# Kernel tuning notes

Measured on AMD Instinct MI355X. Metric: run time of the kernel, lower is better.

Reference implementation:

```python
import jax, jax.numpy as jnp
import numpy as np

DIM = 384
NUM_HEADS = 12
HEAD_DIM = 32
MID = NUM_HEADS * HEAD_DIM
RES = (32, 32)


def _relative_position_index(res):
    Hh, Ww = res
    coords = np.stack(np.meshgrid(np.arange(Hh), np.arange(Ww), indexing='ij'))  # 2,H,W
    cf = coords.reshape(2, -1)
    rel = cf[:, :, None] - cf[:, None, :]  # 2,N,N
    rel = rel.transpose(1, 2, 0).astype(np.int64)
    rel[:, :, 0] += Hh - 1
    rel[:, :, 1] += Ww - 1
    rel[:, :, 0] *= 2 * Ww - 1
    return rel.sum(-1)  # N,N


def setup_inputs() -> dict:
    key = jax.random.key(0)
    ks = jax.random.split(key, 8)
    B = 8
    Hh, Ww = RES
    table_size = (2 * Hh - 1) * (2 * Ww - 1)
    x = jax.random.normal(ks[0], (B, DIM, Hh, Ww), dtype=jnp.float32)
    wq = jax.random.normal(ks[1], (MID, DIM), dtype=jnp.float32) * 0.02
    bq = jnp.zeros((MID,), dtype=jnp.float32)
    wkv = jax.random.normal(ks[2], (2 * MID, DIM), dtype=jnp.float32) * 0.02
    bkv = jnp.zeros((2 * MID,), dtype=jnp.float32)
    wproj = jax.random.normal(ks[3], (DIM, MID), dtype=jnp.float32) * 0.02
    bproj = jnp.zeros((DIM,), dtype=jnp.float32)
    bias_table = jax.random.normal(ks[4], (table_size, NUM_HEADS), dtype=jnp.float32) * 0.02
    rel_index = jnp.asarray(_relative_position_index(RES), dtype=jnp.int32)  # N,N
    return {"x": x, "wq": wq, "bq": bq, "wkv": wkv, "bkv": bkv,
            "wproj": wproj, "bproj": bproj, "bias_table": bias_table,
            "rel_index": rel_index}


def reference(x, wq, bq, wkv, bkv, wproj, bproj, bias_table, rel_index):
    B, C, Hh, Ww = x.shape
    N = Hh * Ww
    scale = HEAD_DIM ** -0.5
    xf = x.reshape(B, C, N)  # B,C,N
    # 1x1 convs == channelwise linear
    q = jnp.einsum('oc,bcn->bon', wq, xf) + bq[None, :, None]          # B,MID,N
    kv = jnp.einsum('oc,bcn->bon', wkv, xf) + bkv[None, :, None]       # B,2*MID,N
    q = q.reshape(B, NUM_HEADS, HEAD_DIM, N).transpose(0, 1, 3, 2)     # B,h,N,d
    kv = kv.reshape(B, 2, NUM_HEADS, HEAD_DIM, N)
    k = kv[:, 0].transpose(0, 1, 3, 2)                                  # B,h,N,d
    v = kv[:, 1].transpose(0, 1, 3, 2)                                  # B,h,N,d
    attn = jnp.einsum('bhnd,bhmd->bhnm', q, k) * scale                  # B,h,N,N
    rel_bias = bias_table[rel_index.reshape(-1)].reshape(N, N, NUM_HEADS)
    attn = attn + rel_bias.transpose(2, 0, 1)[None]                     # + h,N,N bias
    attn = jax.nn.softmax(attn, axis=-1)
    out = jnp.einsum('bhnm,bhmd->bhnd', attn, v)                        # B,h,N,d
    out = out.transpose(0, 1, 3, 2).reshape(B, MID, N)                  # B,MID,N
    out = jnp.einsum('om,bmn->bon', wproj, out) + bproj[None, :, None]  # B,DIM,N
    return out.reshape(B, C, Hh, Ww)
```

## Files before the change

kernel.cpp:

```cpp
#include <hip/hip_runtime.h>

typedef __bf16 bf16;
typedef __bf16 bf16x8 __attribute__((ext_vector_type(8)));
typedef __bf16 bf16x4 __attribute__((ext_vector_type(4)));
typedef float  f32x4  __attribute__((ext_vector_type(4)));

static constexpr int NB = 8;
static constexpr int NH = 12;
static constexpr int HD = 32;
static constexpr int NN = 1024;
static constexpr int NC = 384;
static constexpr int NTBL = 3969;

static constexpr float LOG2E = 1.4426950408889634f;
static constexpr float QSC   = (float)(0.17677669529663687 * 1.4426950408889634);

static constexpr size_t XT_N   = (size_t)NB*NN*NC;
static constexpr size_t WQKV_N = (size_t)3*NC*NC;
static constexpr size_t WP_N   = (size_t)NC*NC;
static constexpr size_t QKV_N  = (size_t)NB*NH*NN*HD;

static constexpr size_t XT_OFF   = 0;
static constexpr size_t WQKV_OFF = XT_OFF + XT_N;
static constexpr size_t WP_OFF   = WQKV_OFF + WQKV_N;
static constexpr size_t Q_OFF    = WP_OFF + WP_N;
static constexpr size_t K_OFF    = Q_OFF + QKV_N;
static constexpr size_t V_OFF    = K_OFF + QKV_N;
static constexpr size_t AO_OFF   = V_OFF + QKV_N;

#define MFMA16(a,b,c) __builtin_amdgcn_mfma_f32_16x16x32_bf16(a,b,c,0,0,0)

static __device__ inline float fast_exp2(float x) {
#if __has_builtin(__builtin_amdgcn_exp2f)
    return __builtin_amdgcn_exp2f(x);
#else
    return exp2f(x);
#endif
}

__global__ __launch_bounds__(256) void cast_all_kernel(const float* __restrict__ x,
                                                       const float* __restrict__ wq,
                                                       const float* __restrict__ wkv,
                                                       const float* __restrict__ wproj,
                                                       bf16* __restrict__ xt,
                                                       bf16* __restrict__ wqkv,
                                                       bf16* __restrict__ wp)
{
    __shared__ bf16 T[64][68];
    const int t = threadIdx.x;
    if (blockIdx.x >= 768) {
        const size_t i = ((size_t)(blockIdx.x - 768) * 256 + t) * 4;
        if (i >= WQKV_N + WP_N) return;
        const float* src; bf16* dst;
        if (i < (size_t)NC*NC)      { src = wq + i;                     dst = wqkv + i; }
        else if (i < WQKV_N)        { src = wkv + (i - (size_t)NC*NC);  dst = wqkv + i; }
        else                        { src = wproj + (i - WQKV_N);       dst = wp + (i - WQKV_N); }
        float4 v = *(const float4*)src;
        bf16x4 o; o[0] = (bf16)v.x; o[1] = (bf16)v.y; o[2] = (bf16)v.z; o[3] = (bf16)v.w;
        *(bf16x4*)dst = o;
        return;
    }
    const int bid = blockIdx.x;
    const int b = bid / 96, rem = bid % 96, ct = rem >> 4, nt = rem & 15;
    const int c0 = ct * 64, n0 = nt * 64;
    const float* Xb = x + (size_t)b * NC * NN;
    const int nl = t & 63, c4 = (t >> 6) * 4;
#pragma unroll
    for (int i = 0; i < 4; ++i) {
        const int c = c4 + i * 16;
        bf16x4 v;
#pragma unroll
        for (int j = 0; j < 4; ++j)
            v[j] = (bf16)Xb[(size_t)(c0 + c + j) * NN + n0 + nl];
        *(bf16x4*)&T[nl][c] = v;
    }
    __syncthreads();
    const int n = t >> 2;
#pragma unroll
    for (int i = 0; i < 2; ++i) {
        const int cg = (t & 3) * 8 + i * 32;
        bf16x4 a = *(const bf16x4*)&T[n][cg];
        bf16x4 bv = *(const bf16x4*)&T[n][cg + 4];
        bf16x8 vv = __builtin_shufflevector(a, bv, 0, 1, 2, 3, 4, 5, 6, 7);
        *(bf16x8*)&xt[((size_t)b * NN + n0 + n) * NC + c0 + cg] = vv;
    }
}

__global__ __launch_bounds__(256) void qkv_gemm_kernel(
    const bf16* __restrict__ W, const bf16* __restrict__ Xt,
    const float* __restrict__ bq, const float* __restrict__ bkv,
    bf16* __restrict__ Qd, bf16* __restrict__ Kd, bf16* __restrict__ Vd)
{
    __shared__ bf16 As[128][40];
    __shared__ bf16 Bs[128][40];
    const int t = threadIdx.x;
    const int w = t >> 6, lane = t & 63, g = lane >> 4, l16 = lane & 15;
    const int wm = w >> 1, wn = w & 1;
    const int n0g = blockIdx.x * 128;
    const int b = n0g >> 10, n0 = n0g & 1023;
    const int o0 = blockIdx.y * 128;
    const bf16* Xb = Xt + (size_t)b * NN * NC;

    const int sr = t >> 1, sc2 = (t & 1) * 16;

    f32x4 acc[4][4] = {};

    bf16x8 aw[2], bw[2];
#pragma unroll
    for (int i = 0; i < 2; ++i) {
        aw[i] = *(const bf16x8*)&W [(size_t)(o0 + sr) * NC + sc2 + 8*i];
        bw[i] = *(const bf16x8*)&Xb[(size_t)(n0 + sr) * NC + sc2 + 8*i];
    }

    for (int k0 = 0; k0 < NC; k0 += 32) {
        __syncthreads();
#pragma unroll
        for (int i = 0; i < 2; ++i) {
            *(bf16x8*)&As[sr][sc2 + 8*i] = aw[i];
            *(bf16x8*)&Bs[sr][sc2 + 8*i] = bw[i];
        }
        __syncthreads();
        if (k0 + 32 < NC) {
#pragma unroll
            for (int i = 0; i < 2; ++i) {
                aw[i] = *(const bf16x8*)&W [(size_t)(o0 + sr) * NC + k0 + 32 + sc2 + 8*i];
                bw[i] = *(const bf16x8*)&Xb[(size_t)(n0 + sr) * NC + k0 + 32 + sc2 + 8*i];
            }
        }
        bf16x8 a[4], bb[4];
#pragma unroll
        for (int s = 0; s < 4; ++s) {
            a[s]  = *(const bf16x8*)&As[wm*64 + s*16 + l16][g*8];
            bb[s] = *(const bf16x8*)&Bs[wn*64 + s*16 + l16][g*8];
        }
#pragma unroll
        for (int sm = 0; sm < 4; ++sm)
#pragma unroll
            for (int sn = 0; sn < 4; ++sn)
                acc[sm][sn] = MFMA16(a[sm], bb[sn], acc[sm][sn]);
    }

#pragma unroll
    for (int sm = 0; sm < 4; ++sm)
#pragma unroll
    for (int sn = 0; sn < 4; ++sn) {
        const int col   = n0 + wn*64 + sn*16 + l16;
        const int obase = o0 + wm*64 + sm*16 + g*4;
        f32x4 v = acc[sm][sn];
        if (obase < 384) {
            const int hh = obase >> 5, d = obase & 31;
            bf16x4 o4;
#pragma unroll
            for (int r = 0; r < 4; ++r) o4[r] = (bf16)((v[r] + bq[obase + r]) * QSC);
            *(bf16x4*)&Qd[(((size_t)b*NH + hh)*NN + col)*HD + d] = o4;
        } else if (obase < 768) {
            const int oo = obase - 384; const int hh = oo >> 5, d = oo & 31;
            bf16x4 o4;
#pragma unroll
            for (int r = 0; r < 4; ++r) o4[r] = (bf16)(v[r] + bkv[oo + r]);
            *(bf16x4*)&Kd[(((size_t)b*NH + hh)*NN + col)*HD + d] = o4;
        } else {
            const int oo = obase - 768; const int hh = oo >> 5, d = oo & 31;
#pragma unroll
            for (int r = 0; r < 4; ++r)
                Vd[(((size_t)b*NH + hh)*HD + d + r)*NN + col] = (bf16)(v[r] + bkv[obase - 384 + r]);
        }
    }
}

__global__ __launch_bounds__(512, 8) void attn_kernel(
    const bf16* __restrict__ Qg, const bf16* __restrict__ Kg, const bf16* __restrict__ Vg,
    const float* __restrict__ bias_table, bf16* __restrict__ AOt)
{
    __shared__ unsigned int pairTu[63][63];
    __shared__ bf16 Ks[128][40];
    __shared__ bf16 Vs[2][32][72];

    const int t = threadIdx.x;
    const int w = t >> 6, lane = t & 63, g = lane >> 4, l16 = lane & 15;

    const int bid = blockIdx.x;
    const int nid = (bid & 7) * 96 + (bid >> 3);
    const int qt = nid & 7;
    const int hb = nid >> 3;
    const int h = hb % 12, b = hb / 12;

    const bf16* Qb = Qg + ((size_t)(b*NH + h)) * NN * HD;
    const bf16* Kb = Kg + ((size_t)(b*NH + h)) * NN * HD;
    const bf16* Vb = Vg + ((size_t)(b*NH + h)) * HD * NN;

    const int kr = t >> 2, kc2 = (t & 3) * 8;
    const int vd = t >> 4, vmi = (t & 15) * 8;
    const int vsub = vmi >> 6, vmm = vmi & 63;
    const int vqa = ((vmm >> 5) & 1) * 32 + ((vmm >> 2) & 3) * 8 + ((vmm >> 4) & 1) * 4;

    bf16x8 sregK = *(const bf16x8*)&Kb[(size_t)kr * HD + kc2];
    bf16x8 sregV = *(const bf16x8*)&Vb[(size_t)vd * NN + vmi];

    const int q0 = qt * 128;
    const int n_s = q0 + w*16 + l16;
    const bf16x8 qfrag = *(const bf16x8*)&Qb[(size_t)n_s * HD + g*8];

    for (int idx = t; idx < 63 * 62; idx += 512) {
        const int dj = idx / 62, dip = idx % 62;
        bf16 lo = (bf16)(bias_table[(size_t)((dip + 1) * 63 + dj) * NH + h] * LOG2E);
        bf16 hi = (bf16)(bias_table[(size_t)(dip * 63 + dj) * NH + h] * LOG2E);
        pairTu[dj][dip] = (unsigned)__builtin_bit_cast(unsigned short, lo)
                        | ((unsigned)__builtin_bit_cast(unsigned short, hi) << 16);
    }

    const int i1w = (q0 >> 5) + (w >> 1);
    const int j1 = ((w & 1) << 4) | l16;
    const int jA63 = (j1 + 31 - 4*g) * 63;

    bf16x8 vones;
#pragma unroll
    for (int e = 0; e < 8; ++e) vones[e] = (bf16)1.0f;

    f32x4 oacc[2] = {};
    f32x4 oacc_l = {};

    for (int ph = 0; ph < 8; ++ph) {
        __syncthreads();
        *(bf16x8*)&Ks[kr][kc2] = sregK;
        { bf16x4 vlo = __builtin_shufflevector(sregV, sregV, 0, 1, 2, 3);
          bf16x4 vhi = __builtin_shufflevector(sregV, sregV, 4, 5, 6, 7);
          *(bf16x4*)&Vs[vsub][vd][vqa]     = vlo;
          *(bf16x4*)&Vs[vsub][vd][vqa + 8] = vhi; }
        __syncthreads();
        if (ph < 7) {
            const int m1 = (ph + 1) * 128;
            sregK = *(const bf16x8*)&Kb[(size_t)(m1 + kr) * HD + kc2];
            sregV = *(const bf16x8*)&Vb[(size_t)vd * NN + m1 + vmi];
        }

#pragma unroll
        for (int sub = 0; sub < 2; ++sub) {
            const int it = 2 * ph + sub;
            const bf16 (*Vsp)[72] = Vs[sub];
            const int dip = i1w - 2*it + 30;
            const unsigned* pAp = &pairTu[0][0] + jA63 + dip;

            f32x4 bacc[4];
#pragma unroll
            for (int r = 0; r < 4; ++r) {
                const unsigned prA = pAp[-63 * r];
                const unsigned prB = pAp[-63 * r - 1008];
                bacc[0][r] = __uint_as_float(prA << 16);
                bacc[2][r] = __uint_as_float(prA & 0xFFFF0000u);
                bacc[1][r] = __uint_as_float(prB << 16);
                bacc[3][r] = __uint_as_float(prB & 0xFFFF0000u);
            }

            float p[4][4];
#pragma unroll
            for (int sc = 0; sc < 4; ++sc) {
                bf16x8 kf = *(const bf16x8*)&Ks[sub*64 + sc*16 + l16][g*8];
                f32x4 z = MFMA16(kf, qfrag, bacc[sc]);
#pragma unroll
                for (int r = 0; r < 4; ++r) p[sc][r] = fast_exp2(z[r]);
            }

#pragma unroll
            for (int kc = 0; kc < 2; ++kc) {
                bf16x8 pa;
#pragma unroll
                for (int r = 0; r < 4; ++r) {
                    pa[r]     = (bf16)p[2*kc][r];
                    pa[4 + r] = (bf16)p[2*kc + 1][r];
                }
#pragma unroll
                for (int ds = 0; ds < 2; ++ds) {
                    bf16x8 vf = *(const bf16x8*)&Vsp[ds*16 + l16][kc*32 + 8*g];
                    oacc[ds] = MFMA16(pa, vf, oacc[ds]);
                }
                oacc_l = MFMA16(pa, vones, oacc_l);
            }
        }
    }

    float rin[4];
#pragma unroll
    for (int r = 0; r < 4; ++r) rin[r] = 1.0f / oacc_l[r];

    const int nrow = q0 + w*16 + g*4;
#pragma unroll
    for (int ds = 0; ds < 2; ++ds) {
        const int c = h*HD + ds*16 + l16;
#pragma unroll
        for (int r = 0; r < 4; ++r)
            AOt[((size_t)b*NN + nrow + r) * NC + c] = (bf16)(oacc[ds][r] * rin[r]);
    }
}

__global__ __launch_bounds__(256) void proj_gemm_kernel(
    const bf16* __restrict__ W, const bf16* __restrict__ AOt,
    const float* __restrict__ bproj, float* __restrict__ out)
{
    __shared__ bf16 As[64][40];
    __shared__ bf16 Bs[128][40];
    const int t = threadIdx.x;
    const int w = t >> 6, lane = t & 63, g = lane >> 4, l16 = lane & 15;
    const int wm = w >> 1, wn = w & 1;
    const int n0g = blockIdx.x * 128;
    const int b = n0g >> 10, n0 = n0g & 1023;
    const int o0 = blockIdx.y * 64;
    const bf16* Ab = AOt + (size_t)b * NN * NC;

    const int ar = t >> 2, ac = (t & 3) * 8;

    f32x4 acc[2][4] = {};

    bf16x8 aw = *(const bf16x8*)&W[(size_t)(o0 + ar) * NC + ac];
    bf16x8 bw[2];
#pragma unroll
    for (int i = 0; i < 2; ++i) {
        const int s = t + i * 256, r = s >> 2, cc = (s & 3) * 8;
        bw[i] = *(const bf16x8*)&Ab[(size_t)(n0 + r) * NC + cc];
    }

    for (int k0 = 0; k0 < NC; k0 += 32) {
        __syncthreads();
        *(bf16x8*)&As[ar][ac] = aw;
#pragma unroll
        for (int i = 0; i < 2; ++i) {
            const int s = t + i * 256, r = s >> 2, cc = (s & 3) * 8;
            *(bf16x8*)&Bs[r][cc] = bw[i];
        }
        __syncthreads();
        if (k0 + 32 < NC) {
            aw = *(const bf16x8*)&W[(size_t)(o0 + ar) * NC + k0 + 32 + ac];
#pragma unroll
            for (int i = 0; i < 2; ++i) {
                const int s = t + i * 256, r = s >> 2, cc = (s & 3) * 8;
                bw[i] = *(const bf16x8*)&Ab[(size_t)(n0 + r) * NC + k0 + 32 + cc];
            }
        }
        bf16x8 a0 = *(const bf16x8*)&As[wm*32      + l16][g*8];
        bf16x8 a1 = *(const bf16x8*)&As[wm*32 + 16 + l16][g*8];
#pragma unroll
        for (int sn = 0; sn < 4; ++sn) {
            bf16x8 bf = *(const bf16x8*)&Bs[wn*64 + sn*16 + l16][g*8];
            acc[0][sn] = MFMA16(a0, bf, acc[0][sn]);
            acc[1][sn] = MFMA16(a1, bf, acc[1][sn]);
        }
    }

#pragma unroll
    for (int sm = 0; sm < 2; ++sm)
#pragma unroll
    for (int sn = 0; sn < 4; ++sn) {
        const int col   = n0 + wn*64 + sn*16 + l16;
        const int obase = o0 + wm*32 + sm*16 + g*4;
        f32x4 v = acc[sm][sn];
#pragma unroll
        for (int r = 0; r < 4; ++r)
            out[((size_t)b*NC + obase + r)*NN + col] = v[r] + bproj[obase + r];
    }
}

extern "C" void kernel_launch(void* const* d_in, const int* in_sizes, int n_in,
                              void* d_out, int out_size, void* d_ws, size_t ws_size,
                              hipStream_t stream)
{
    const float* x          = (const float*)d_in[0];
    const float* wq         = (const float*)d_in[1];
    const float* bq         = (const float*)d_in[2];
    const float* wkv        = (const float*)d_in[3];
    const float* bkv        = (const float*)d_in[4];
    const float* wproj      = (const float*)d_in[5];
    const float* bproj      = (const float*)d_in[6];
    const float* bias_table = (const float*)d_in[7];
    float* out = (float*)d_out;

    bf16* wsb  = (bf16*)d_ws;
    bf16* Xt   = wsb + XT_OFF;
    bf16* Wqkv = wsb + WQKV_OFF;
    bf16* Wp   = wsb + WP_OFF;
    bf16* Qd   = wsb + Q_OFF;
    bf16* Kd   = wsb + K_OFF;
    bf16* Vd   = wsb + V_OFF;
    bf16* AOt  = wsb + AO_OFF;

    cast_all_kernel<<<dim3(768 + 576), 256, 0, stream>>>(x, wq, wkv, wproj, Xt, Wqkv, Wp);
    qkv_gemm_kernel<<<dim3(64, 9), 256, 0, stream>>>(Wqkv, Xt, bq, bkv, Qd, Kd, Vd);
    attn_kernel<<<dim3(768), 512, 0, stream>>>(Qd, Kd, Vd, bias_table, AOt);
    proj_gemm_kernel<<<dim3(64, 6), 256, 0, stream>>>(Wp, AOt, bproj, out);
}
```

Baseline: 68.50 us.

## Process two query row-tiles per wave and shrink bias table to per-tile window

The attention kernel now runs with 256 threads per block, and each wave handles 32 query rows as two 16-row MFMA tiles. The two tiles share the K and V fragment loads and overlapping bias words from shared memory. The relative-position bias table kept in LDS is cut to the 34-column window that this query tile needs, which reduces table-building work and LDS footprint. The trade-off is more accumulator registers per thread and fewer waves per block, which may lower occupancy and latency hiding.

```diff
diff --git a/kernel.cpp b/kernel.cpp
--- a/kernel.cpp
+++ b/kernel.cpp
@@ -168,11 +168,11 @@
     }
 }
 
-__global__ __launch_bounds__(512, 8) void attn_kernel(
+__global__ __launch_bounds__(256, 4) void attn_kernel(
     const bf16* __restrict__ Qg, const bf16* __restrict__ Kg, const bf16* __restrict__ Vg,
     const float* __restrict__ bias_table, bf16* __restrict__ AOt)
 {
-    __shared__ unsigned int pairTu[63][63];
+    __shared__ unsigned int pairTw[63][34];
     __shared__ bf16 Ks[128][40];
     __shared__ bf16 Vs[2][32][72];
 
@@ -189,107 +189,133 @@
     const bf16* Kb = Kg + ((size_t)(b*NH + h)) * NN * HD;
     const bf16* Vb = Vg + ((size_t)(b*NH + h)) * HD * NN;
 
-    const int kr = t >> 2, kc2 = (t & 3) * 8;
-    const int vd = t >> 4, vmi = (t & 15) * 8;
-    const int vsub = vmi >> 6, vmm = vmi & 63;
-    const int vqa = ((vmm >> 5) & 1) * 32 + ((vmm >> 2) & 3) * 8 + ((vmm >> 4) & 1) * 4;
-
-    bf16x8 sregK = *(const bf16x8*)&Kb[(size_t)kr * HD + kc2];
-    bf16x8 sregV = *(const bf16x8*)&Vb[(size_t)vd * NN + vmi];
+    const int kr = t >> 1, kc2 = (t & 1) * 16;
+    const int vd = t >> 3, vmb = (t & 7) * 16;
+    int vsub[2], vqa[2];
+#pragma unroll
+    for (int i = 0; i < 2; ++i) {
+        const int vm = vmb + 8*i, vmm = vm & 63;
+        vsub[i] = vm >> 6;
+        vqa[i]  = ((vmm >> 5) & 1) * 32 + ((vmm >> 2) & 3) * 8 + ((vmm >> 4) & 1) * 4;
+    }
+
+    bf16x8 sregK[2], sregV[2];
+#pragma unroll
+    for (int i = 0; i < 2; ++i) {
+        sregK[i] = *(const bf16x8*)&Kb[(size_t)kr * HD + kc2 + 8*i];
+        sregV[i] = *(const bf16x8*)&Vb[(size_t)vd * NN + vmb + 8*i];
+    }
 
     const int q0 = qt * 128;
-    const int n_s = q0 + w*16 + l16;
-    const bf16x8 qfrag = *(const bf16x8*)&Qb[(size_t)n_s * HD + g*8];
-
-    for (int idx = t; idx < 63 * 62; idx += 512) {
-        const int dj = idx / 62, dip = idx % 62;
+    const bf16x8 qfrag0 = *(const bf16x8*)&Qb[(size_t)(q0 + w*32      + l16) * HD + g*8];
+    const bf16x8 qfrag1 = *(const bf16x8*)&Qb[(size_t)(q0 + w*32 + 16 + l16) * HD + g*8];
+
+    for (int idx = t; idx < 63 * 34; idx += 256) {
+        const int dj = idx / 34, dipl = idx % 34;
+        const int dip = dipl + 4 * qt;
         bf16 lo = (bf16)(bias_table[(size_t)((dip + 1) * 63 + dj) * NH + h] * LOG2E);
         bf16 hi = (bf16)(bias_table[(size_t)(dip * 63 + dj) * NH + h] * LOG2E);
-        pairTu[dj][dip] = (unsigned)__builtin_bit_cast(unsigned short, lo)
-                        | ((unsigned)__builtin_bit_cast(unsigned short, hi) << 16);
-    }
-
-    const int i1w = (q0 >> 5) + (w >> 1);
-    const int j1 = ((w & 1) << 4) | l16;
-    const int jA63 = (j1 + 31 - 4*g) * 63;
+        pairTw[dj][dipl] = (unsigned)__builtin_bit_cast(unsigned short, lo)
+                         | ((unsigned)__builtin_bit_cast(unsigned short, hi) << 16);
+    }
+
+    const unsigned* twp = &pairTw[0][0];
+    const int rowD1 = (l16 + 31 - 4*g) * 34;
 
     bf16x8 vones;
 #pragma unroll
     for (int e = 0; e < 8; ++e) vones[e] = (bf16)1.0f;
 
-    f32x4 oacc[2] = {};
-    f32x4 oacc_l = {};
+    f32x4 oacc0[2] = {}, oacc1[2] = {};
+    f32x4 oacc_l0 = {}, oacc_l1 = {};
 
     for (int ph = 0; ph < 8; ++ph) {
         __syncthreads();
-        *(bf16x8*)&Ks[kr][kc2] = sregK;
-        { bf16x4 vlo = __builtin_shufflevector(sregV, sregV, 0, 1, 2, 3);
-          bf16x4 vhi = __builtin_shufflevector(sregV, sregV, 4, 5, 6, 7);
-          *(bf16x4*)&Vs[vsub][vd][vqa]     = vlo;
-          *(bf16x4*)&Vs[vsub][vd][vqa + 8] = vhi; }
+#pragma unroll
+        for (int i = 0; i < 2; ++i) {
+            *(bf16x8*)&Ks[kr][kc2 + 8*i] = sregK[i];
+            bf16x4 vlo = __builtin_shufflevector(sregV[i], sregV[i], 0, 1, 2, 3);
+            bf16x4 vhi = __builtin_shufflevector(sregV[i], sregV[i], 4, 5, 6, 7);
+            *(bf16x4*)&Vs[vsub[i]][vd][vqa[i]]     = vlo;
+            *(bf16x4*)&Vs[vsub[i]][vd][vqa[i] + 8] = vhi;
+        }
         __syncthreads();
         if (ph < 7) {
             const int m1 = (ph + 1) * 128;
-            sregK = *(const bf16x8*)&Kb[(size_t)(m1 + kr) * HD + kc2];
-            sregV = *(const bf16x8*)&Vb[(size_t)vd * NN + m1 + vmi];
+#pragma unroll
+            for (int i = 0; i < 2; ++i) {
+                sregK[i] = *(const bf16x8*)&Kb[(size_t)(m1 + kr) * HD + kc2 + 8*i];
+                sregV[i] = *(const bf16x8*)&Vb[(size_t)vd * NN + m1 + vmb + 8*i];
+            }
         }
 
 #pragma unroll
         for (int sub = 0; sub < 2; ++sub) {
             const int it = 2 * ph + sub;
             const bf16 (*Vsp)[72] = Vs[sub];
-            const int dip = i1w - 2*it + 30;
-            const unsigned* pAp = &pairTu[0][0] + jA63 + dip;
-
-            f32x4 bacc[4];
+            const int dipl = w + 30 - 2*it;
+            const unsigned* pD1 = twp + rowD1 + dipl;
+
+            f32x4 b00, b01, b02, b03, b10, b12;
 #pragma unroll
             for (int r = 0; r < 4; ++r) {
-                const unsigned prA = pAp[-63 * r];
-                const unsigned prB = pAp[-63 * r - 1008];
-                bacc[0][r] = __uint_as_float(prA << 16);
-                bacc[2][r] = __uint_as_float(prA & 0xFFFF0000u);
-                bacc[1][r] = __uint_as_float(prB << 16);
-                bacc[3][r] = __uint_as_float(prB & 0xFFFF0000u);
-            }
-
-            float p[4][4];
+                const unsigned d1w = pD1[-34 * r];
+                const unsigned d0w = pD1[-34 * r - 544];
+                const unsigned d2w = pD1[-34 * r + 544];
+                b00[r] = __uint_as_float(d1w << 16);
+                b02[r] = __uint_as_float(d1w & 0xFFFF0000u);
+                b01[r] = __uint_as_float(d0w << 16);
+                b03[r] = __uint_as_float(d0w & 0xFFFF0000u);
+                b10[r] = __uint_as_float(d2w << 16);
+                b12[r] = __uint_as_float(d2w & 0xFFFF0000u);
+            }
+            f32x4 bacc0[4] = {b00, b01, b02, b03};
+            f32x4 bacc1[4] = {b10, b00, b12, b02};
+
+            bf16x8 pa0[2], pa1[2];
 #pragma unroll
             for (int sc = 0; sc < 4; ++sc) {
                 bf16x8 kf = *(const bf16x8*)&Ks[sub*64 + sc*16 + l16][g*8];
-                f32x4 z = MFMA16(kf, qfrag, bacc[sc]);
-#pragma unroll
-                for (int r = 0; r < 4; ++r) p[sc][r] = fast_exp2(z[r]);
+                f32x4 z0 = MFMA16(kf, qfrag0, bacc0[sc]);
+                f32x4 z1 = MFMA16(kf, qfrag1, bacc1[sc]);
+                const int kc = sc >> 1, hl = (sc & 1) * 4;
+#pragma unroll
+                for (int r = 0; r < 4; ++r) {
+                    pa0[kc][hl + r] = (bf16)fast_exp2(z0[r]);
+                    pa1[kc][hl + r] = (bf16)fast_exp2(z1[r]);
+                }
             }
 
 #pragma unroll
             for (int kc = 0; kc < 2; ++kc) {
-                bf16x8 pa;
-#pragma unroll
-                for (int r = 0; r < 4; ++r) {
-                    pa[r]     = (bf16)p[2*kc][r];
-                    pa[4 + r] = (bf16)p[2*kc + 1][r];
-                }
 #pragma unroll
                 for (int ds = 0; ds < 2; ++ds) {
                     bf16x8 vf = *(const bf16x8*)&Vsp[ds*16 + l16][kc*32 + 8*g];
-                    oacc[ds] = MFMA16(pa, vf, oacc[ds]);
+                    oacc0[ds] = MFMA16(pa0[kc], vf, oacc0[ds]);
+                    oacc1[ds] = MFMA16(pa1[kc], vf, oacc1[ds]);
                 }
-                oacc_l = MFMA16(pa, vones, oacc_l);
-            }
-        }
-    }
-
-    float rin[4];
-#pragma unroll
-    for (int r = 0; r < 4; ++r) rin[r] = 1.0f / oacc_l[r];
-
-    const int nrow = q0 + w*16 + g*4;
+                oacc_l0 = MFMA16(pa0[kc], vones, oacc_l0);
+                oacc_l1 = MFMA16(pa1[kc], vones, oacc_l1);
+            }
+        }
+    }
+
+    float rin0[4], rin1[4];
+#pragma unroll
+    for (int r = 0; r < 4; ++r) {
+        rin0[r] = 1.0f / oacc_l0[r];
+        rin1[r] = 1.0f / oacc_l1[r];
+    }
+
+    const int nrow0 = q0 + w*32 + g*4;
 #pragma unroll
     for (int ds = 0; ds < 2; ++ds) {
         const int c = h*HD + ds*16 + l16;
 #pragma unroll
-        for (int r = 0; r < 4; ++r)
-            AOt[((size_t)b*NN + nrow + r) * NC + c] = (bf16)(oacc[ds][r] * rin[r]);
+        for (int r = 0; r < 4; ++r) {
+            AOt[((size_t)b*NN + nrow0 + r)      * NC + c] = (bf16)(oacc0[ds][r] * rin0[r]);
+            AOt[((size_t)b*NN + nrow0 + 16 + r) * NC + c] = (bf16)(oacc1[ds][r] * rin1[r]);
+        }
     }
 }
 
@@ -384,6 +410,6 @@
 
     cast_all_kernel<<<dim3(768 + 576), 256, 0, stream>>>(x, wq, wkv, wproj, Xt, Wqkv, Wp);
     qkv_gemm_kernel<<<dim3(64, 9), 256, 0, stream>>>(Wqkv, Xt, bq, bkv, Qd, Kd, Vd);
-    attn_kernel<<<dim3(768), 512, 0, stream>>>(Qd, Kd, Vd, bias_table, AOt);
+    attn_kernel<<<dim3(768), 256, 0, stream>>>(Qd, Kd, Vd, bias_table, AOt);
     proj_gemm_kernel<<<dim3(64, 6), 256, 0, stream>>>(Wp, AOt, bproj, out);
 }
```

After: 66.26 us. 1.03x faster.
